# Performance work log

Hardware: AMD Instinct MI355X
Metric: run time of the kernel (lower is better)

The kernel has to match this reference:

```python
import jax, jax.numpy as jnp
import numpy as np

DIM, DIM_KQ, DIM_V, N = 1024, 64, 64, 8192

def setup_inputs() -> dict:
    key = jax.random.key(0)
    kx, kq, kk, kv = jax.random.split(key, 4)
    x = jax.random.normal(kx, (N, DIM), dtype=jnp.float32)
    # original uses torch.rand (uniform [0,1)) for parameter init
    w_q = jax.random.uniform(kq, (DIM, DIM_KQ), dtype=jnp.float32)
    w_k = jax.random.uniform(kk, (DIM, DIM_KQ), dtype=jnp.float32)
    w_v = jax.random.uniform(kv, (DIM, DIM_V), dtype=jnp.float32)
    return {"x": x, "w_q": w_q, "w_k": w_k, "w_v": w_v}

def reference(x, w_q, w_k, w_v):
    q = x @ w_q            # [N, dkq]
    k = x @ w_k            # [N, dkq]
    v = x @ w_v            # [N, dv]
    scale = 1.0 / jnp.sqrt(jnp.asarray(DIM_KQ, dtype=x.dtype))
    att_s = (q @ k.T) * scale           # [N, N]
    att_w = jax.nn.softmax(att_s, axis=-1)
    return att_w @ v                    # [N, dv]
```

## Files before the change

### kernel.cpp

```cpp
#include <hip/hip_runtime.h>
#include <hip/hip_bf16.h>
#include <math.h>

constexpr int N    = 8192;
constexpr int DIM  = 1024;

typedef __attribute__((ext_vector_type(8))) short bf16x8;
typedef __attribute__((ext_vector_type(4))) float f32x4;

__device__ inline unsigned short f2bf(float f) {
    unsigned u = __float_as_uint(f);
    u += 0x7fffu + ((u >> 16) & 1u);
    return (unsigned short)(u >> 16);
}
__device__ inline float bf2f(unsigned short h) {
    return __uint_as_float((unsigned)h << 16);
}
__device__ inline void gload16(const void* gsrc, void* ldst) {
    typedef __attribute__((address_space(1))) const unsigned int GU;
    typedef __attribute__((address_space(3))) unsigned int LU;
    __builtin_amdgcn_global_load_lds((GU*)gsrc, (LU*)ldst, 16, 0, 0);
}

__global__ __launch_bounds__(256) void prep_w_kernel(
    const float* __restrict__ wq, const float* __restrict__ wk,
    const float* __restrict__ wv,
    unsigned short* __restrict__ wthi, unsigned short* __restrict__ wtlo)
{
    int idx = blockIdx.x * 256 + threadIdx.x;
    int c   = idx >> 10;
    int k   = idx & 1023;
    const float* wsrc = (c < 64) ? wq : (c < 128) ? wk : wv;
    float f = wsrc[(size_t)k * 64 + (c & 63)];
    unsigned short h = f2bf(f);
    int pos = c * 1024 + (k & ~63) + ((((k >> 3) & 7) ^ (c & 7)) << 3) + (k & 7);
    wthi[pos] = h;
    wtlo[pos] = f2bf(f - bf2f(h));
}

__global__ __launch_bounds__(256) void proj_kernel(
    const float* __restrict__ x,
    const unsigned short* __restrict__ wthi,
    const unsigned short* __restrict__ wtlo,
    unsigned short* __restrict__ qhi, unsigned short* __restrict__ qlo,
    unsigned short* __restrict__ khi, unsigned short* __restrict__ klo,
    unsigned short* __restrict__ vthi)
{
    __shared__ unsigned short As[2][2][4096];
    __shared__ unsigned short Bs[2][2][3072];

    const int tid  = threadIdx.x;
    const int lane = tid & 63;
    const int w    = tid >> 6;
    const int g16  = lane >> 4;
    const int i16  = lane & 15;
    const int row0 = blockIdx.x * 64;
    const int col0 = blockIdx.y * 48;

    float4 xn[4];
    auto loadX = [&](int t) {
#pragma unroll
        for (int i = 0; i < 4; ++i) {
            int f4 = i * 256 + tid;
            xn[i] = *reinterpret_cast<const float4*>(
                x + (size_t)(row0 + (f4 >> 4)) * DIM + t * 64 + (f4 & 15) * 4);
        }
    };
    auto stageB = [&](int t, int buf) {
#pragma unroll
        for (int i = 0; i < 3; ++i) {
            int idx = i * 256 + tid;
            int p   = (idx >= 384) ? 1 : 0;
            int li  = idx - p * 384;
            const unsigned short* base = p ? wtlo : wthi;
            const unsigned short* src  = base + (size_t)(col0 + (li >> 3)) * 1024
                                         + t * 64 + (li & 7) * 8;
            gload16(src, (char*)&Bs[buf][p][0] + (size_t)li * 16);
        }
    };
    auto writeA = [&](int buf) {
#pragma unroll
        for (int i = 0; i < 4; ++i) {
            int f4 = i * 256 + tid;
            int r = f4 >> 4, c4 = f4 & 15;
            float4 v = xn[i];
            unsigned short h0 = f2bf(v.x), h1 = f2bf(v.y),
                           h2 = f2bf(v.z), h3 = f2bf(v.w);
            unsigned short l0 = f2bf(v.x - bf2f(h0)), l1 = f2bf(v.y - bf2f(h1)),
                           l2 = f2bf(v.z - bf2f(h2)), l3 = f2bf(v.w - bf2f(h3));
            uint2 uh = { (unsigned)h0 | ((unsigned)h1 << 16),
                         (unsigned)h2 | ((unsigned)h3 << 16) };
            uint2 ul = { (unsigned)l0 | ((unsigned)l1 << 16),
                         (unsigned)l2 | ((unsigned)l3 << 16) };
            int byte = r * 128 + (((c4 >> 1) ^ (r & 7)) << 4) + ((c4 & 1) << 3);
            *reinterpret_cast<uint2*>((char*)&As[buf][0][0] + byte) = uh;
            *reinterpret_cast<uint2*>((char*)&As[buf][1][0] + byte) = ul;
        }
    };

    f32x4 acc[3];
    acc[0] = acc[1] = acc[2] = (f32x4){0.f, 0.f, 0.f, 0.f};

    loadX(0);
    stageB(0, 0);
    writeA(0);

    const int arow = w * 16 + i16;
    for (int t = 0; t < 16; ++t) {
        const int b = t & 1;
        __syncthreads();
        if (t < 15) {
            loadX(t + 1);
            stageB(t + 1, b ^ 1);
        }
        bf16x8 ah[2], al[2];
#pragma unroll
        for (int kc = 0; kc < 2; ++kc) {
            int off = arow * 128 + ((((kc << 2) | g16) ^ (arow & 7)) << 4);
            ah[kc] = *reinterpret_cast<const bf16x8*>((char*)&As[b][0][0] + off);
            al[kc] = *reinterpret_cast<const bf16x8*>((char*)&As[b][1][0] + off);
        }
#pragma unroll
        for (int ct = 0; ct < 3; ++ct) {
            const int colL = ct * 16 + i16;
#pragma unroll
            for (int kc = 0; kc < 2; ++kc) {
                int off = colL * 128 + ((((kc << 2) | g16) ^ (colL & 7)) << 4);
                bf16x8 bh = *reinterpret_cast<const bf16x8*>((char*)&Bs[b][0][0] + off);
                bf16x8 bl = *reinterpret_cast<const bf16x8*>((char*)&Bs[b][1][0] + off);
                acc[ct] = __builtin_amdgcn_mfma_f32_16x16x32_bf16(ah[kc], bh, acc[ct], 0, 0, 0);
                acc[ct] = __builtin_amdgcn_mfma_f32_16x16x32_bf16(ah[kc], bl, acc[ct], 0, 0, 0);
                acc[ct] = __builtin_amdgcn_mfma_f32_16x16x32_bf16(al[kc], bh, acc[ct], 0, 0, 0);
            }
        }
        if (t < 15) writeA(b ^ 1);
    }

    const float QSCALE = 0.180336880f;
#pragma unroll
    for (int ct = 0; ct < 3; ++ct) {
        int cglob = col0 + ct * 16 + i16;
        int g = cglob >> 6, c64 = cglob & 63;
#pragma unroll
        for (int rr = 0; rr < 4; ++rr) {
            int row = row0 + w * 16 + 4 * g16 + rr;
            float f = acc[ct][rr];
            if (g == 0) {
                f *= QSCALE;
                unsigned short h = f2bf(f);
                qhi[(size_t)row * 64 + c64] = h;
                qlo[(size_t)row * 64 + c64] = f2bf(f - bf2f(h));
            } else if (g == 1) {
                int ci = c64 ^ ((row & 7) << 3);
                unsigned short h = f2bf(f);
                khi[(size_t)row * 64 + ci] = h;
                klo[(size_t)row * 64 + ci] = f2bf(f - bf2f(h));
            } else {
                int cg  = row >> 3;
                int cgs = (cg & ~7) | ((cg & 7) ^ (c64 & 7));
                vthi[(size_t)c64 * 8192 + cgs * 8 + (row & 7)] = f2bf(f);
            }
        }
    }
}

constexpr int BQ = 64;
constexpr int BK = 64;

__global__ __launch_bounds__(256) void attn_kernel(
    const unsigned short* __restrict__ qhi, const unsigned short* __restrict__ qlo,
    const unsigned short* __restrict__ khi, const unsigned short* __restrict__ klo,
    const unsigned short* __restrict__ vthi,
    float* __restrict__ po, float* __restrict__ pm, float* __restrict__ pl,
    int keys_per_split)
{
    __shared__ __align__(16) unsigned short stage[12288];
    __shared__ __align__(16) unsigned short plds[4][1024];

    const int tid  = threadIdx.x;
    const int lane = tid & 63;
    const int w    = tid >> 6;
    const int g16  = lane >> 4;
    const int i16  = lane & 15;
    const int qrow0 = blockIdx.x * BQ;
    const int split = blockIdx.y;
    const int key0  = split * keys_per_split;
    const int nt    = keys_per_split / BK;

    bf16x8 qh[2], ql[2];
    {
        const size_t qr = (size_t)(qrow0 + w * 16 + i16) * 64;
#pragma unroll
        for (int c = 0; c < 2; ++c) {
            qh[c] = *reinterpret_cast<const bf16x8*>(qhi + qr + c * 32 + g16 * 8);
            ql[c] = *reinterpret_cast<const bf16x8*>(qlo + qr + c * 32 + g16 * 8);
        }
    }

    float m = -INFINITY;
    float l = 0.f;
    f32x4 o_acc[4];
#pragma unroll
    for (int db = 0; db < 4; ++db) o_acc[db] = {0.f, 0.f, 0.f, 0.f};

    char* pb = (char*)&plds[w][0];
    const int wbase = i16 * 128;

    for (int t = 0; t < nt; ++t) {
        const int key0t = key0 + t * BK;
        __syncthreads();
#pragma unroll
        for (int u = 0; u < 6; ++u) {
            int row = ((u & 1) << 5) + (tid >> 3);
            int ch  = tid & 7;
            const unsigned short* src;
            if (u < 2)      src = khi  + (size_t)(key0t + row) * 64 + ch * 8;
            else if (u < 4) src = klo  + (size_t)(key0t + row) * 64 + ch * 8;
            else            src = vthi + (size_t)row * 8192 + key0t + ch * 8;
            gload16(src, (char*)stage + u * 4096 + tid * 16);
        }
        __syncthreads();
        const char* stg = (const char*)stage;

        f32x4 sacc[4];
#pragma unroll
        for (int j = 0; j < 4; ++j) {
            f32x4 a = {0.f, 0.f, 0.f, 0.f};
            const int kr = 16 * j + i16;
#pragma unroll
            for (int c = 0; c < 2; ++c) {
                const int byteO = kr * 128 + ((c * 64 + g16 * 16) ^ ((kr & 7) << 4));
                bf16x8 kh = *reinterpret_cast<const bf16x8*>(stg + byteO);
                bf16x8 kl = *reinterpret_cast<const bf16x8*>(stg + byteO + 8192);
                a = __builtin_amdgcn_mfma_f32_16x16x32_bf16(kh, qh[c], a, 0, 0, 0);
                a = __builtin_amdgcn_mfma_f32_16x16x32_bf16(kh, ql[c], a, 0, 0, 0);
                a = __builtin_amdgcn_mfma_f32_16x16x32_bf16(kl, qh[c], a, 0, 0, 0);
            }
            sacc[j] = a;
        }

        float aloc = sacc[0][0];
#pragma unroll
        for (int j = 0; j < 4; ++j)
#pragma unroll
            for (int r = 0; r < 4; ++r) aloc = fmaxf(aloc, sacc[j][r]);
        if (__any(aloc > m + 8.f)) {
            float a2 = fmaxf(aloc, __shfl_xor(aloc, 16));
            a2 = fmaxf(a2, __shfl_xor(a2, 32));
            float mn   = fmaxf(m, a2);
            float corr = exp2f(m - mn);
            m = mn;
            l *= corr;
#pragma unroll
            for (int db = 0; db < 4; ++db) o_acc[db] *= corr;
        }

#pragma unroll
        for (int j = 0; j < 4; ++j) {
            float p0 = exp2f(sacc[j][0] - m);
            float p1 = exp2f(sacc[j][1] - m);
            float p2 = exp2f(sacc[j][2] - m);
            float p3 = exp2f(sacc[j][3] - m);
            l += (p0 + p1) + (p2 + p3);
            uint2 pdw = { (unsigned)f2bf(p0) | ((unsigned)f2bf(p1) << 16),
                          (unsigned)f2bf(p2) | ((unsigned)f2bf(p3) << 16) };
            int off = wbase + ((32 * j + 8 * g16) ^ ((i16 & 7) << 4));
            *reinterpret_cast<uint2*>(pb + off) = pdw;
        }

        bf16x8 pfrag[2];
#pragma unroll
        for (int c = 0; c < 2; ++c) {
            int off = wbase + ((64 * c + 16 * g16) ^ ((i16 & 7) << 4));
            pfrag[c] = *reinterpret_cast<const bf16x8*>(pb + off);
        }
#pragma unroll
        for (int db = 0; db < 4; ++db) {
            f32x4 a = o_acc[db];
            const int vr = 16 * db + i16;
#pragma unroll
            for (int c = 0; c < 2; ++c) {
                const int byteO = 16384 + vr * 128 +
                                  ((c * 64 + g16 * 16) ^ ((vr & 7) << 4));
                bf16x8 vh = *reinterpret_cast<const bf16x8*>(stg + byteO);
                a = __builtin_amdgcn_mfma_f32_16x16x32_bf16(vh, pfrag[c], a, 0, 0, 0);
            }
            o_acc[db] = a;
        }
    }

    l += __shfl_xor(l, 16);
    l += __shfl_xor(l, 32);
    const size_t prow = (size_t)split * N + qrow0 + w * 16;
#pragma unroll
    for (int db = 0; db < 4; ++db) {
        float4 ov = {o_acc[db][0], o_acc[db][1], o_acc[db][2], o_acc[db][3]};
        *reinterpret_cast<float4*>(po + (prow + i16) * 64 + 16 * db + 4 * g16) = ov;
    }
    if (lane < 16) {
        pm[prow + i16] = m;
        pl[prow + i16] = l;
    }
}

__global__ __launch_bounds__(256) void combine_kernel(
    const float* __restrict__ po,
    const float* __restrict__ pm,
    const float* __restrict__ pl,
    float* __restrict__ out, int ns)
{
    const int tid = threadIdx.x;
    const int row = blockIdx.x * 16 + (tid >> 4);
    const int c4  = tid & 15;

    float M = -INFINITY;
    for (int s = 0; s < ns; ++s)
        M = fmaxf(M, pm[(size_t)s * N + row]);
    float L = 0.f;
    float4 acc = {0.f, 0.f, 0.f, 0.f};
    for (int s = 0; s < ns; ++s) {
        float ws = exp2f(pm[(size_t)s * N + row] - M);
        L += ws * pl[(size_t)s * N + row];
        float4 ov = *reinterpret_cast<const float4*>(
            po + ((size_t)s * N + row) * 64 + c4 * 4);
        acc.x += ws * ov.x; acc.y += ws * ov.y;
        acc.z += ws * ov.z; acc.w += ws * ov.w;
    }
    float inv = 1.f / L;
    float4 res = {acc.x * inv, acc.y * inv, acc.z * inv, acc.w * inv};
    *reinterpret_cast<float4*>(out + (size_t)row * 64 + c4 * 4) = res;
}

extern "C" void kernel_launch(void* const* d_in, const int* in_sizes, int n_in,
                              void* d_out, int out_size, void* d_ws, size_t ws_size,
                              hipStream_t stream)
{
    const float* x  = (const float*)d_in[0];
    const float* wq = (const float*)d_in[1];
    const float* wk = (const float*)d_in[2];
    const float* wv = (const float*)d_in[3];
    float* out = (float*)d_out;

    const size_t PLANE = (size_t)N * 64;
    unsigned short* qhi  = (unsigned short*)d_ws;
    unsigned short* qlo  = qhi + PLANE;
    unsigned short* khi  = qlo + PLANE;
    unsigned short* klo  = khi + PLANE;
    unsigned short* vthi = klo + PLANE;
    const size_t plane_bytes = 5 * PLANE * 2;
    const size_t wt_elems = (size_t)192 * 1024;
    const size_t wt_bytes = 2 * wt_elems * 2;

    int ns = 8;
    while (ns > 1 &&
           plane_bytes + wt_bytes +
           (size_t)ns * ((size_t)N * 64 * 4 + (size_t)N * 8) > ws_size)
        ns >>= 1;

    float* po = (float*)((char*)d_ws + plane_bytes);
    float* pm = po + (size_t)ns * N * 64;
    float* pl = pm + (size_t)ns * N;
    unsigned short* wthi = (unsigned short*)(pl + (size_t)ns * N);
    unsigned short* wtlo = wthi + wt_elems;

    prep_w_kernel<<<768, 256, 0, stream>>>(wq, wk, wv, wthi, wtlo);

    dim3 pgrid(N / 64, 4);
    proj_kernel<<<pgrid, 256, 0, stream>>>(x, wthi, wtlo,
                                           qhi, qlo, khi, klo, vthi);

    dim3 agrid(N / BQ, ns);
    attn_kernel<<<agrid, 256, 0, stream>>>(qhi, qlo, khi, klo, vthi,
                                           po, pm, pl, N / ns);

    combine_kernel<<<N / 16, 256, 0, stream>>>(po, pm, pl, out, ns);
}
```

Before: 93.87 us.

## Use hardware bf16 pack conversion and deepen X prefetch in projection GEMM

Replaces the software round-to-nearest bf16 conversion with the packed v_cvt_pk_bf16_f32 instruction, both in the hi/lo split of x and in packing softmax probabilities. It also double-buffers the x register prefetch so global loads are issued two k-steps ahead, and fully unrolls the projection k-loop. The max reduction in attention is rewritten as a balanced tree to shorten the dependency chain. The cost is more registers held for the extra prefetch stage, which may lower occupancy.

Result: faster. 85.39 us (-9.0%).

```diff
diff --git a/kernel.cpp b/kernel.cpp
--- a/kernel.cpp
+++ b/kernel.cpp
@@ -15,6 +15,11 @@
 }
 __device__ inline float bf2f(unsigned short h) {
     return __uint_as_float((unsigned)h << 16);
+}
+__device__ inline unsigned cvtpk(float a, float b) {
+    unsigned r;
+    asm("v_cvt_pk_bf16_f32 %0, %1, %2" : "=v"(r) : "v"(a), "v"(b));
+    return r;
 }
 __device__ inline void gload16(const void* gsrc, void* ldst) {
     typedef __attribute__((address_space(1))) const unsigned int GU;
@@ -57,12 +62,12 @@
     const int row0 = blockIdx.x * 64;
     const int col0 = blockIdx.y * 48;
 
-    float4 xn[4];
-    auto loadX = [&](int t) {
+    float4 xn[2][4];
+    auto loadX = [&](int t, int s) {
 #pragma unroll
         for (int i = 0; i < 4; ++i) {
             int f4 = i * 256 + tid;
-            xn[i] = *reinterpret_cast<const float4*>(
+            xn[s][i] = *reinterpret_cast<const float4*>(
                 x + (size_t)(row0 + (f4 >> 4)) * DIM + t * 64 + (f4 & 15) * 4);
         }
     };
@@ -78,20 +83,20 @@
             gload16(src, (char*)&Bs[buf][p][0] + (size_t)li * 16);
         }
     };
-    auto writeA = [&](int buf) {
+    auto writeA = [&](int buf, int s) {
 #pragma unroll
         for (int i = 0; i < 4; ++i) {
             int f4 = i * 256 + tid;
             int r = f4 >> 4, c4 = f4 & 15;
-            float4 v = xn[i];
-            unsigned short h0 = f2bf(v.x), h1 = f2bf(v.y),
-                           h2 = f2bf(v.z), h3 = f2bf(v.w);
-            unsigned short l0 = f2bf(v.x - bf2f(h0)), l1 = f2bf(v.y - bf2f(h1)),
-                           l2 = f2bf(v.z - bf2f(h2)), l3 = f2bf(v.w - bf2f(h3));
-            uint2 uh = { (unsigned)h0 | ((unsigned)h1 << 16),
-                         (unsigned)h2 | ((unsigned)h3 << 16) };
-            uint2 ul = { (unsigned)l0 | ((unsigned)l1 << 16),
-                         (unsigned)l2 | ((unsigned)l3 << 16) };
+            float4 v = xn[s][i];
+            unsigned h01 = cvtpk(v.x, v.y);
+            unsigned h23 = cvtpk(v.z, v.w);
+            float hx = __uint_as_float(h01 << 16);
+            float hy = __uint_as_float(h01 & 0xffff0000u);
+            float hz = __uint_as_float(h23 << 16);
+            float hw = __uint_as_float(h23 & 0xffff0000u);
+            uint2 uh = { h01, h23 };
+            uint2 ul = { cvtpk(v.x - hx, v.y - hy), cvtpk(v.z - hz, v.w - hw) };
             int byte = r * 128 + (((c4 >> 1) ^ (r & 7)) << 4) + ((c4 & 1) << 3);
             *reinterpret_cast<uint2*>((char*)&As[buf][0][0] + byte) = uh;
             *reinterpret_cast<uint2*>((char*)&As[buf][1][0] + byte) = ul;
@@ -101,18 +106,18 @@
     f32x4 acc[3];
     acc[0] = acc[1] = acc[2] = (f32x4){0.f, 0.f, 0.f, 0.f};
 
-    loadX(0);
+    loadX(0, 0);
+    loadX(1, 1);
     stageB(0, 0);
-    writeA(0);
+    writeA(0, 0);
 
     const int arow = w * 16 + i16;
+#pragma unroll
     for (int t = 0; t < 16; ++t) {
         const int b = t & 1;
         __syncthreads();
-        if (t < 15) {
-            loadX(t + 1);
-            stageB(t + 1, b ^ 1);
-        }
+        if (t < 15) stageB(t + 1, b ^ 1);
+        if (t < 14) loadX(t + 2, b);
         bf16x8 ah[2], al[2];
 #pragma unroll
         for (int kc = 0; kc < 2; ++kc) {
@@ -133,7 +138,7 @@
                 acc[ct] = __builtin_amdgcn_mfma_f32_16x16x32_bf16(al[kc], bh, acc[ct], 0, 0, 0);
             }
         }
-        if (t < 15) writeA(b ^ 1);
+        if (t < 15) writeA(b ^ 1, b ^ 1);
     }
 
     const float QSCALE = 0.180336880f;
@@ -239,15 +244,15 @@
             sacc[j] = a;
         }
 
-        float aloc = sacc[0][0];
-#pragma unroll
-        for (int j = 0; j < 4; ++j)
-#pragma unroll
-            for (int r = 0; r < 4; ++r) aloc = fmaxf(aloc, sacc[j][r]);
+        float a0 = fmaxf(fmaxf(sacc[0][0], sacc[0][1]), fmaxf(sacc[0][2], sacc[0][3]));
+        float a1 = fmaxf(fmaxf(sacc[1][0], sacc[1][1]), fmaxf(sacc[1][2], sacc[1][3]));
+        float a2 = fmaxf(fmaxf(sacc[2][0], sacc[2][1]), fmaxf(sacc[2][2], sacc[2][3]));
+        float a3 = fmaxf(fmaxf(sacc[3][0], sacc[3][1]), fmaxf(sacc[3][2], sacc[3][3]));
+        float aloc = fmaxf(fmaxf(a0, a1), fmaxf(a2, a3));
         if (__any(aloc > m + 8.f)) {
-            float a2 = fmaxf(aloc, __shfl_xor(aloc, 16));
-            a2 = fmaxf(a2, __shfl_xor(a2, 32));
-            float mn   = fmaxf(m, a2);
+            float x2 = fmaxf(aloc, __shfl_xor(aloc, 16));
+            x2 = fmaxf(x2, __shfl_xor(x2, 32));
+            float mn   = fmaxf(m, x2);
             float corr = exp2f(m - mn);
             m = mn;
             l *= corr;
@@ -262,8 +267,7 @@
             float p2 = exp2f(sacc[j][2] - m);
             float p3 = exp2f(sacc[j][3] - m);
             l += (p0 + p1) + (p2 + p3);
-            uint2 pdw = { (unsigned)f2bf(p0) | ((unsigned)f2bf(p1) << 16),
-                          (unsigned)f2bf(p2) | ((unsigned)f2bf(p3) << 16) };
+            uint2 pdw = { cvtpk(p0, p1), cvtpk(p2, p3) };
             int off = wbase + ((32 * j + 8 * g16) ^ ((i16 & 7) << 4));
             *reinterpret_cast<uint2*>(pb + off) = pdw;
         }
```
